# Kernel tuning notes

Measured on AMD Instinct MI355X. Metric: run time of the kernel, lower is better.

## Reference

```python
import jax, jax.numpy as jnp
import numpy as np

B, T, C, H = 2, 2048, 1024, 16
D = C // H  # head dim = 64
NEG_MIN = jnp.finfo(jnp.float32).min


def setup_inputs() -> dict:
    key = jax.random.key(0)
    ks = jax.random.split(key, 5)
    std = 0.02
    return {
        "x": jax.random.normal(ks[0], (B, T, C), dtype=jnp.float32),
        "Wq": std * jax.random.normal(ks[1], (C, C), dtype=jnp.float32),
        "bq": jnp.zeros((C,), dtype=jnp.float32),
        "Wk": std * jax.random.normal(ks[2], (C, C), dtype=jnp.float32),
        "bk": jnp.zeros((C,), dtype=jnp.float32),
        "Wv": std * jax.random.normal(ks[3], (C, C), dtype=jnp.float32),
        "bv": jnp.zeros((C,), dtype=jnp.float32),
        "Wo": (std / np.sqrt(24.0)) * jax.random.normal(ks[4], (C, C), dtype=jnp.float32),
        "bo": jnp.zeros((C,), dtype=jnp.float32),
    }


def reference(x, Wq, bq, Wk, bk, Wv, bv, Wo, bo):
    # QKV projections -> (B, H, T, D)
    def proj(W, b):
        return (x @ W + b).reshape(B, T, H, D).transpose(0, 2, 1, 3)

    q = proj(Wq, bq)
    k = proj(Wk, bk)
    v = proj(Wv, bv)

    # full scores (B, H, T, T), causal mask, softmax
    attn = jnp.einsum("bhqd,bhkd->bhqk", q, k) / jnp.sqrt(jnp.float32(D))
    mask = jnp.tril(jnp.ones((T, T), dtype=bool))[None, None]
    attn = jnp.where(mask, attn, NEG_MIN)
    scores = jax.nn.softmax(attn, axis=-1)

    out = jnp.einsum("bhqk,bhkd->bhqd", scores, v)
    out = out.transpose(0, 2, 1, 3).reshape(B, T, C)
    return out @ Wo + bo
```

## Files before the change

kernel.cpp:

```cpp
#include <hip/hip_runtime.h>
#include <stdint.h>
#include <stddef.h>


#define B_SZ 2
#define T_SZ 2048
#define C_SZ 1024
#define H_SZ 16
#define D_SZ 64
#define M_SZ (B_SZ * T_SZ)
#define BHTD (B_SZ * H_SZ * T_SZ * D_SZ)
#define CC (C_SZ * C_SZ)

typedef __attribute__((ext_vector_type(8))) __bf16 bf16x8;
typedef __attribute__((ext_vector_type(4))) float f32x4;
typedef __attribute__((ext_vector_type(16))) float f32x16;

__device__ __forceinline__ unsigned short f2bf(float f) {
    union { float f; unsigned u; } v; v.f = f;
    v.u += 0x7fffu + ((v.u >> 16) & 1u);
    return (unsigned short)(v.u >> 16);
}

__device__ __forceinline__ unsigned pkbf(float lo, float hi_) {
    union { unsigned u; __bf16 h[2]; } r;
    r.h[0] = (__bf16)lo; r.h[1] = (__bf16)hi_;
    return r.u;
}

__device__ __forceinline__ void load_lds16(const unsigned short* g, unsigned short* l) {
    __builtin_amdgcn_global_load_lds(
        (const __attribute__((address_space(1))) void*)g,
        (__attribute__((address_space(3))) void*)l, 16, 0, 0);
}


__global__ void cvt_x_kernel(const float4* __restrict__ in, ushort4* __restrict__ out, int n4) {
    int stride = gridDim.x * blockDim.x;
    for (int i = blockIdx.x * blockDim.x + threadIdx.x; i < n4; i += stride) {
        float4 v = in[i];
        ushort4 o;
        o.x = f2bf(v.x); o.y = f2bf(v.y); o.z = f2bf(v.z); o.w = f2bf(v.w);
        out[i] = o;
    }
}

__global__ __launch_bounds__(256) void transpose_cvt_kernel(
    const float* __restrict__ W0, const float* __restrict__ W1,
    const float* __restrict__ W2, const float* __restrict__ W3,
    unsigned short* __restrict__ T0, unsigned short* __restrict__ T1,
    unsigned short* __restrict__ T2, unsigned short* __restrict__ T3)
{
    __shared__ float tile[32][33];
    const float* W; unsigned short* Wt;
    switch (blockIdx.z) {
        case 0: W = W0; Wt = T0; break;
        case 1: W = W1; Wt = T1; break;
        case 2: W = W2; Wt = T2; break;
        default: W = W3; Wt = T3; break;
    }
    const int tx = threadIdx.x, ty = threadIdx.y;
    const int n0 = blockIdx.x * 32, k0 = blockIdx.y * 32;
    #pragma unroll
    for (int i = 0; i < 4; i++)
        tile[ty + i * 8][tx] = W[(size_t)(k0 + ty + i * 8) * C_SZ + n0 + tx];
    __syncthreads();
    #pragma unroll
    for (int i = 0; i < 4; i++)
        Wt[(size_t)(n0 + ty + i * 8) * C_SZ + k0 + tx] = f2bf(tile[tx][ty + i * 8]);
}

__global__ __launch_bounds__(256) void vt_kernel(
    const unsigned short* __restrict__ V, unsigned short* __restrict__ Vt)
{
    __shared__ unsigned short tile[32][33];
    const int bh = blockIdx.z;
    const int t0 = blockIdx.x * 32, d0 = blockIdx.y * 32;
    const unsigned short* src = V + (size_t)bh * T_SZ * D_SZ;
    unsigned short* dst = Vt + (size_t)bh * T_SZ * D_SZ;
    const int tx = threadIdx.x, ty = threadIdx.y;
    #pragma unroll
    for (int i = 0; i < 4; i++)
        tile[ty + i * 8][tx] = src[(size_t)(t0 + ty + i * 8) * D_SZ + d0 + tx];
    __syncthreads();
    #pragma unroll
    for (int i = 0; i < 4; i++)
        dst[(size_t)(d0 + ty + i * 8) * T_SZ + t0 + tx] = tile[tx][ty + i * 8];
}


__device__ __forceinline__ void gemm_tile_core(
    const unsigned short* __restrict__ A,
    const unsigned short* __restrict__ Bt,
    unsigned short* As, unsigned short* Bs,
    int m0, int n0, f32x4 acc[4][4])
{
    const int tid = threadIdx.x;
    const int lane = tid & 63;
    const int w = tid >> 6;
    const int l15 = lane & 15, lg = lane >> 4;
    const int wr = (w >> 1) * 64, wc = (w & 1) * 64;

    const unsigned short* Ag0 = A + (size_t)(m0 + (tid >> 2)) * C_SZ + (tid & 3) * 8;
    const unsigned short* Ag1 = Ag0 + (size_t)64 * C_SZ;
    const unsigned short* Bg0 = Bt + (size_t)(n0 + (tid >> 2)) * C_SZ + (tid & 3) * 8;
    const unsigned short* Bg1 = Bg0 + (size_t)64 * C_SZ;
    unsigned short* As0 = As + w * 512;
    unsigned short* As1 = As + 2048 + w * 512;
    unsigned short* Bs0 = Bs + w * 512;
    unsigned short* Bs1 = Bs + 2048 + w * 512;

    for (int k0 = 0; k0 < C_SZ; k0 += 32) {
        load_lds16(Ag0 + k0, As0);
        load_lds16(Ag1 + k0, As1);
        load_lds16(Bg0 + k0, Bs0);
        load_lds16(Bg1 + k0, Bs1);
        __syncthreads();
        bf16x8 af[4], bfv[4];
        const bf16x8* Ap = (const bf16x8*)As;
        const bf16x8* Bp = (const bf16x8*)Bs;
        #pragma unroll
        for (int m = 0; m < 4; m++) af[m] = Ap[(wr + m * 16 + l15) * 4 + lg];
        #pragma unroll
        for (int n = 0; n < 4; n++) bfv[n] = Bp[(wc + n * 16 + l15) * 4 + lg];
        #pragma unroll
        for (int m = 0; m < 4; m++)
            #pragma unroll
            for (int n = 0; n < 4; n++)
                acc[m][n] = __builtin_amdgcn_mfma_f32_16x16x32_bf16(af[m], bfv[n], acc[m][n], 0, 0, 0);
        __syncthreads();
    }
}

__global__ __launch_bounds__(256) void gemm_qkv_kernel(
    const unsigned short* __restrict__ A,
    const unsigned short* __restrict__ WtBase,
    const float* __restrict__ bq, const float* __restrict__ bk, const float* __restrict__ bv,
    unsigned short* __restrict__ QKV, unsigned short* __restrict__ Vtmp)
{
    __shared__ unsigned short As[4096], Bs[4096];
    const int z = blockIdx.z;
    const unsigned short* Bt = WtBase + (size_t)z * CC;
    const float* bias = (z == 0) ? bq : (z == 1) ? bk : bv;
    const float scale = (z == 0) ? 0.18033688011112042f : 1.0f;
    unsigned short* Out = (z == 2) ? Vtmp : QKV + (size_t)z * BHTD;

    f32x4 acc[4][4];
    f32x4 zero4 = {0.f, 0.f, 0.f, 0.f};
    #pragma unroll
    for (int m = 0; m < 4; m++)
        #pragma unroll
        for (int n = 0; n < 4; n++) acc[m][n] = zero4;

    const int m0 = blockIdx.y * 128, n0 = blockIdx.x * 128;
    gemm_tile_core(A, Bt, As, Bs, m0, n0, acc);

    const int lane = threadIdx.x & 63;
    const int w = threadIdx.x >> 6;
    const int l15 = lane & 15, lg = lane >> 4;
    const int wr = (w >> 1) * 64, wc = (w & 1) * 64;
    #pragma unroll
    for (int n = 0; n < 4; n++) {
        const int col = n0 + wc + n * 16 + l15;
        const float bias_v = bias[col];
        const int h = col >> 6, d = col & 63;
        #pragma unroll
        for (int m = 0; m < 4; m++) {
            #pragma unroll
            for (int j = 0; j < 4; j++) {
                const int row = m0 + wr + m * 16 + lg * 4 + j;
                const int b = row >> 11, t = row & (T_SZ - 1);
                Out[(((size_t)(b * H_SZ + h)) * T_SZ + t) * D_SZ + d] =
                    f2bf((acc[m][n][j] + bias_v) * scale);
            }
        }
    }
}

__global__ __launch_bounds__(256) void gemm_out_kernel(
    const unsigned short* __restrict__ A,
    const unsigned short* __restrict__ Bt,
    const float* __restrict__ bo,
    float* __restrict__ Out)
{
    __shared__ unsigned short As[4096], Bs[4096];
    f32x4 acc[4][4];
    f32x4 zero4 = {0.f, 0.f, 0.f, 0.f};
    #pragma unroll
    for (int m = 0; m < 4; m++)
        #pragma unroll
        for (int n = 0; n < 4; n++) acc[m][n] = zero4;

    const int m0 = blockIdx.y * 128, n0 = blockIdx.x * 128;
    gemm_tile_core(A, Bt, As, Bs, m0, n0, acc);

    const int lane = threadIdx.x & 63;
    const int w = threadIdx.x >> 6;
    const int l15 = lane & 15, lg = lane >> 4;
    const int wr = (w >> 1) * 64, wc = (w & 1) * 64;
    #pragma unroll
    for (int n = 0; n < 4; n++) {
        const int col = n0 + wc + n * 16 + l15;
        const float bias_v = bo[col];
        #pragma unroll
        for (int m = 0; m < 4; m++) {
            #pragma unroll
            for (int j = 0; j < 4; j++) {
                const int row = m0 + wr + m * 16 + lg * 4 + j;
                Out[(size_t)row * C_SZ + col] = acc[m][n][j] + bias_v;
            }
        }
    }
}

__global__ __launch_bounds__(256) void attn_fwd_kernel(
    const unsigned short* __restrict__ Q,
    const unsigned short* __restrict__ K,
    const unsigned short* __restrict__ Vt,
    unsigned short* __restrict__ O)
{
    const int idx = blockIdx.x;
    const int qt = (idx < 256) ? (15 - (idx >> 5)) : ((idx - 256) >> 5);
    const int bh = idx & 31;
    const int w = threadIdx.x >> 6;
    const int lane = threadIdx.x & 63;
    const int l31 = lane & 31, hi = lane >> 5;
    const int qw = qt * 128 + 32 * w;

    const unsigned short* Qh = Q + (size_t)bh * T_SZ * D_SZ;
    const unsigned short* Kh = K + (size_t)bh * T_SZ * D_SZ;
    const unsigned short* Vh = Vt + (size_t)bh * T_SZ * D_SZ;

    __shared__ __align__(16) unsigned short smem[16384];

    const int c0 = w * 64 + lane;
    const int row0 = c0 >> 3;
    const int sw0 = (c0 & 7) ^ (row0 & 7);
    const int koff0 = row0 * 64 + sw0 * 8;
    const int voff0 = row0 * T_SZ + sw0 * 8;
    const int ldsb0 = w * 512;

    bf16x8 qf[4];
    #pragma unroll
    for (int j = 0; j < 4; j++)
        qf[j] = *(const bf16x8*)&Qh[(size_t)(qw + l31) * D_SZ + j * 16 + 8 * hi];

    f32x16 acc[2];
    #pragma unroll
    for (int r = 0; r < 16; r++) { acc[0][r] = 0.f; acc[1][r] = 0.f; }
    float mrun = -3.0e38f, lrun = 0.f;

    const int tlast = (qw + 31) >> 6;
    const int ntb = 2 * qt + 2;
    const int qrow = qw + l31;
    const int swl = l31 & 7;

    load_lds16(Kh + koff0, smem + ldsb0);
    load_lds16(Kh + koff0 + 2048, smem + 2048 + ldsb0);
    load_lds16(Vh + voff0, smem + 4096 + ldsb0);
    load_lds16(Vh + voff0 + 32 * T_SZ, smem + 6144 + ldsb0);

    for (int tt = 0; tt < ntb; ++tt) {
        if (tt + 1 < ntb) {
            unsigned short* Bd = smem + ((tt + 1) & 1) * 8192;
            const unsigned short* Kt = Kh + (size_t)(tt + 1) * 64 * D_SZ;
            const unsigned short* Vtt = Vh + (tt + 1) * 64;
            load_lds16(Kt + koff0, Bd + ldsb0);
            load_lds16(Kt + koff0 + 2048, Bd + 2048 + ldsb0);
            load_lds16(Vtt + voff0, Bd + 4096 + ldsb0);
            load_lds16(Vtt + voff0 + 32 * T_SZ, Bd + 6144 + ldsb0);
            asm volatile("s_waitcnt vmcnt(4)" ::: "memory");
        } else {
            asm volatile("s_waitcnt vmcnt(0)" ::: "memory");
        }
        __builtin_amdgcn_s_barrier();

        if (tt <= tlast) {
            const unsigned short* Ks = smem + (tt & 1) * 8192;
            const unsigned short* Vs = Ks + 4096;
            const int k0 = tt * 64;

            f32x16 s[2];
            #pragma unroll
            for (int kb = 0; kb < 2; ++kb) {
                bf16x8 kf[4];
                #pragma unroll
                for (int j = 0; j < 4; ++j) {
                    const int ch = (j * 2 + hi) ^ swl;
                    kf[j] = *(const bf16x8*)&Ks[(kb * 32 + l31) * 64 + ch * 8];
                }
                f32x16 sc;
                #pragma unroll
                for (int r = 0; r < 16; r++) sc[r] = 0.f;
                #pragma unroll
                for (int j = 0; j < 4; ++j)
                    sc = __builtin_amdgcn_mfma_f32_32x32x16_bf16(kf[j], qf[j], sc, 0, 0, 0);
                s[kb] = sc;
            }

            if (k0 + 63 > qw) {
                #pragma unroll
                for (int kb = 0; kb < 2; ++kb)
                    #pragma unroll
                    for (int r = 0; r < 16; ++r) {
                        const int kv = k0 + kb * 32 + (r & 3) + 8 * (r >> 2) + 4 * hi;
                        s[kb][r] = (kv > qrow) ? -3.0e38f : s[kb][r];
                    }
            }

            float pm = s[0][0];
            #pragma unroll
            for (int r = 1; r < 16; r++) pm = fmaxf(pm, s[0][r]);
            #pragma unroll
            for (int r = 0; r < 16; r++) pm = fmaxf(pm, s[1][r]);
            pm = fmaxf(pm, __shfl_xor(pm, 32));

            if (!__all(pm <= mrun + 8.0f)) {
                const float mnew = fmaxf(mrun, pm);
                const float al = exp2f(mrun - mnew);
                lrun *= al;
                #pragma unroll
                for (int r = 0; r < 16; r++) { acc[0][r] *= al; acc[1][r] *= al; }
                mrun = mnew;
            }

            float ps = 0.f;
            #pragma unroll
            for (int kb = 0; kb < 2; ++kb)
                #pragma unroll
                for (int r = 0; r < 16; r++) { s[kb][r] = exp2f(s[kb][r] - mrun); ps += s[kb][r]; }
            ps += __shfl_xor(ps, 32);
            lrun += ps;

            bf16x8 pf[2][2];
            #pragma unroll
            for (int kb = 0; kb < 2; ++kb) {
                #pragma unroll
                for (int ksl = 0; ksl < 2; ++ksl) {
                    unsigned a0 = pkbf(s[kb][8 * ksl + 0], s[kb][8 * ksl + 1]);
                    unsigned a1 = pkbf(s[kb][8 * ksl + 2], s[kb][8 * ksl + 3]);
                    unsigned b0 = pkbf(s[kb][8 * ksl + 4], s[kb][8 * ksl + 5]);
                    unsigned b1 = pkbf(s[kb][8 * ksl + 6], s[kb][8 * ksl + 7]);
                    asm volatile("v_permlane32_swap_b32 %0, %1" : "+v"(a0), "+v"(b0));
                    asm volatile("v_permlane32_swap_b32 %0, %1" : "+v"(a1), "+v"(b1));
                    union { unsigned u[4]; bf16x8 v; } fr;
                    fr.u[0] = a0; fr.u[1] = a1; fr.u[2] = b0; fr.u[3] = b1;
                    pf[kb][ksl] = fr.v;
                }
            }

            #pragma unroll
            for (int dt = 0; dt < 2; ++dt)
                #pragma unroll
                for (int kb = 0; kb < 2; ++kb)
                    #pragma unroll
                    for (int ksl = 0; ksl < 2; ++ksl) {
                        const int ks = kb * 2 + ksl;
                        const int ch = (ks * 2 + hi) ^ swl;
                        const bf16x8 vf = *(const bf16x8*)&Vs[(dt * 32 + l31) * 64 + ch * 8];
                        acc[dt] = __builtin_amdgcn_mfma_f32_32x32x16_bf16(vf, pf[kb][ksl], acc[dt], 0, 0, 0);
                    }
        }
        __builtin_amdgcn_s_barrier();
    }

    unsigned short* ot = smem + w * 2304;
    const float inv = 1.0f / lrun;
    #pragma unroll
    for (int g = 0; g < 4; g++) {
        ushort4 wa, wb;
        wa.x = f2bf(acc[0][4 * g + 0] * inv); wa.y = f2bf(acc[0][4 * g + 1] * inv);
        wa.z = f2bf(acc[0][4 * g + 2] * inv); wa.w = f2bf(acc[0][4 * g + 3] * inv);
        wb.x = f2bf(acc[1][4 * g + 0] * inv); wb.y = f2bf(acc[1][4 * g + 1] * inv);
        wb.z = f2bf(acc[1][4 * g + 2] * inv); wb.w = f2bf(acc[1][4 * g + 3] * inv);
        *(ushort4*)&ot[l31 * 72 + 8 * g + 4 * hi] = wa;
        *(ushort4*)&ot[l31 * 72 + 32 + 8 * g + 4 * hi] = wb;
    }
    const int b = bh >> 4, h = bh & 15;
    #pragma unroll
    for (int pss = 0; pss < 4; pss++) {
        const int q = pss * 8 + (lane >> 3);
        const uint4 val = *(const uint4*)&ot[q * 72 + (lane & 7) * 8];
        *(uint4*)&O[((size_t)(b * T_SZ + qw + q)) * C_SZ + h * D_SZ + (lane & 7) * 8] = val;
    }
}


extern "C" void kernel_launch(void* const* d_in, const int* in_sizes, int n_in,
                              void* d_out, int out_size, void* d_ws, size_t ws_size,
                              hipStream_t stream)
{
    const float* x  = (const float*)d_in[0];
    const float* Wq = (const float*)d_in[1];
    const float* bq = (const float*)d_in[2];
    const float* Wk = (const float*)d_in[3];
    const float* bk = (const float*)d_in[4];
    const float* Wv = (const float*)d_in[5];
    const float* bv = (const float*)d_in[6];
    const float* Wo = (const float*)d_in[7];
    const float* bo = (const float*)d_in[8];

    uint8_t* ws = (uint8_t*)d_ws;
    unsigned short* XB   = (unsigned short*)(ws);
    unsigned short* WT   = (unsigned short*)(ws + (8u  << 20));
    unsigned short* QKV  = (unsigned short*)(ws + (16u << 20));
    unsigned short* Vtmp = (unsigned short*)(ws + (40u << 20));

    cvt_x_kernel<<<2048, 256, 0, stream>>>((const float4*)x, (ushort4*)XB, M_SZ * C_SZ / 4);
    transpose_cvt_kernel<<<dim3(32, 32, 4), dim3(32, 8), 0, stream>>>(
        Wq, Wk, Wv, Wo, WT, WT + CC, WT + 2 * (size_t)CC, WT + 3 * (size_t)CC);
    gemm_qkv_kernel<<<dim3(8, 32, 3), 256, 0, stream>>>(XB, WT, bq, bk, bv, QKV, Vtmp);
    vt_kernel<<<dim3(64, 2, 32), dim3(32, 8), 0, stream>>>(Vtmp, QKV + 2 * (size_t)BHTD);
    attn_fwd_kernel<<<512, 256, 0, stream>>>(
        QKV, QKV + BHTD, QKV + 2 * (size_t)BHTD, Vtmp);
    gemm_out_kernel<<<dim3(8, 32), 256, 0, stream>>>(Vtmp, WT + 3 * (size_t)CC, bo, (float*)d_out);
}
```

Baseline: 131.8 us.

## Retile output GEMM to 64x128, flatten QKV grid, tree-reduce softmax max/sum

```diff
diff --git a/kernel.cpp b/kernel.cpp
--- a/kernel.cpp
+++ b/kernel.cpp
@@ -139,7 +139,7 @@
     unsigned short* __restrict__ QKV, unsigned short* __restrict__ Vtmp)
 {
     __shared__ unsigned short As[4096], Bs[4096];
-    const int z = blockIdx.z;
+    const int z = blockIdx.x >> 3;
     const unsigned short* Bt = WtBase + (size_t)z * CC;
     const float* bias = (z == 0) ? bq : (z == 1) ? bk : bv;
     const float scale = (z == 0) ? 0.18033688011112042f : 1.0f;
@@ -152,7 +152,7 @@
         #pragma unroll
         for (int n = 0; n < 4; n++) acc[m][n] = zero4;
 
-    const int m0 = blockIdx.y * 128, n0 = blockIdx.x * 128;
+    const int m0 = blockIdx.y * 128, n0 = (blockIdx.x & 7) * 128;
     gemm_tile_core(A, Bt, As, Bs, m0, n0, acc);
 
     const int lane = threadIdx.x & 63;
@@ -183,30 +183,57 @@
     const float* __restrict__ bo,
     float* __restrict__ Out)
 {
-    __shared__ unsigned short As[4096], Bs[4096];
-    f32x4 acc[4][4];
+    __shared__ unsigned short As[2048], Bs[4096];
+    const int tid = threadIdx.x;
+    const int lane = tid & 63;
+    const int w = tid >> 6;
+    const int l15 = lane & 15, lg = lane >> 4;
+    const int wc = w * 32;
+    const int m0 = blockIdx.y * 64, n0 = blockIdx.x * 128;
+
+    const unsigned short* Ag  = A + (size_t)(m0 + (tid >> 2)) * C_SZ + (tid & 3) * 8;
+    const unsigned short* Bg0 = Bt + (size_t)(n0 + (tid >> 2)) * C_SZ + (tid & 3) * 8;
+    const unsigned short* Bg1 = Bg0 + (size_t)64 * C_SZ;
+    unsigned short* As0 = As + w * 512;
+    unsigned short* Bs0 = Bs + w * 512;
+    unsigned short* Bs1 = Bs + 2048 + w * 512;
+
+    f32x4 acc[4][2];
     f32x4 zero4 = {0.f, 0.f, 0.f, 0.f};
     #pragma unroll
     for (int m = 0; m < 4; m++)
         #pragma unroll
-        for (int n = 0; n < 4; n++) acc[m][n] = zero4;
-
-    const int m0 = blockIdx.y * 128, n0 = blockIdx.x * 128;
-    gemm_tile_core(A, Bt, As, Bs, m0, n0, acc);
-
-    const int lane = threadIdx.x & 63;
-    const int w = threadIdx.x >> 6;
-    const int l15 = lane & 15, lg = lane >> 4;
-    const int wr = (w >> 1) * 64, wc = (w & 1) * 64;
-    #pragma unroll
-    for (int n = 0; n < 4; n++) {
+        for (int n = 0; n < 2; n++) acc[m][n] = zero4;
+
+    for (int k0 = 0; k0 < C_SZ; k0 += 32) {
+        load_lds16(Ag + k0, As0);
+        load_lds16(Bg0 + k0, Bs0);
+        load_lds16(Bg1 + k0, Bs1);
+        __syncthreads();
+        bf16x8 af[4], bfv[2];
+        const bf16x8* Ap = (const bf16x8*)As;
+        const bf16x8* Bp = (const bf16x8*)Bs;
+        #pragma unroll
+        for (int m = 0; m < 4; m++) af[m] = Ap[(m * 16 + l15) * 4 + lg];
+        #pragma unroll
+        for (int n = 0; n < 2; n++) bfv[n] = Bp[(wc + n * 16 + l15) * 4 + lg];
+        #pragma unroll
+        for (int m = 0; m < 4; m++)
+            #pragma unroll
+            for (int n = 0; n < 2; n++)
+                acc[m][n] = __builtin_amdgcn_mfma_f32_16x16x32_bf16(af[m], bfv[n], acc[m][n], 0, 0, 0);
+        __syncthreads();
+    }
+
+    #pragma unroll
+    for (int n = 0; n < 2; n++) {
         const int col = n0 + wc + n * 16 + l15;
         const float bias_v = bo[col];
         #pragma unroll
         for (int m = 0; m < 4; m++) {
             #pragma unroll
             for (int j = 0; j < 4; j++) {
-                const int row = m0 + wr + m * 16 + lg * 4 + j;
+                const int row = m0 + m * 16 + lg * 4 + j;
                 Out[(size_t)row * C_SZ + col] = acc[m][n][j] + bias_v;
             }
         }
@@ -308,12 +335,14 @@
                     }
             }
 
-            float pm = s[0][0];
-            #pragma unroll
-            for (int r = 1; r < 16; r++) pm = fmaxf(pm, s[0][r]);
-            #pragma unroll
-            for (int r = 0; r < 16; r++) pm = fmaxf(pm, s[1][r]);
-            pm = fmaxf(pm, __shfl_xor(pm, 32));
+            float t16[16];
+            #pragma unroll
+            for (int i = 0; i < 16; i++) t16[i] = fmaxf(s[0][i], s[1][i]);
+            #pragma unroll
+            for (int st = 8; st >= 1; st >>= 1)
+                #pragma unroll
+                for (int i = 0; i < st; i++) t16[i] = fmaxf(t16[i], t16[i + st]);
+            const float pm = fmaxf(t16[0], __shfl_xor(t16[0], 32));
 
             if (!__all(pm <= mrun + 8.0f)) {
                 const float mnew = fmaxf(mrun, pm);
@@ -324,13 +353,18 @@
                 mrun = mnew;
             }
 
-            float ps = 0.f;
             #pragma unroll
             for (int kb = 0; kb < 2; ++kb)
                 #pragma unroll
-                for (int r = 0; r < 16; r++) { s[kb][r] = exp2f(s[kb][r] - mrun); ps += s[kb][r]; }
-            ps += __shfl_xor(ps, 32);
-            lrun += ps;
+                for (int r = 0; r < 16; r++) s[kb][r] = exp2f(s[kb][r] - mrun);
+            float a16[16];
+            #pragma unroll
+            for (int i = 0; i < 16; i++) a16[i] = s[0][i] + s[1][i];
+            #pragma unroll
+            for (int st = 8; st >= 1; st >>= 1)
+                #pragma unroll
+                for (int i = 0; i < st; i++) a16[i] += a16[i + st];
+            lrun += a16[0] + __shfl_xor(a16[0], 32);
 
             bf16x8 pf[2][2];
             #pragma unroll
@@ -409,9 +443,9 @@
     cvt_x_kernel<<<2048, 256, 0, stream>>>((const float4*)x, (ushort4*)XB, M_SZ * C_SZ / 4);
     transpose_cvt_kernel<<<dim3(32, 32, 4), dim3(32, 8), 0, stream>>>(
         Wq, Wk, Wv, Wo, WT, WT + CC, WT + 2 * (size_t)CC, WT + 3 * (size_t)CC);
-    gemm_qkv_kernel<<<dim3(8, 32, 3), 256, 0, stream>>>(XB, WT, bq, bk, bv, QKV, Vtmp);
+    gemm_qkv_kernel<<<dim3(24, 32), 256, 0, stream>>>(XB, WT, bq, bk, bv, QKV, Vtmp);
     vt_kernel<<<dim3(64, 2, 32), dim3(32, 8), 0, stream>>>(Vtmp, QKV + 2 * (size_t)BHTD);
     attn_fwd_kernel<<<512, 256, 0, stream>>>(
         QKV, QKV + BHTD, QKV + 2 * (size_t)BHTD, Vtmp);
-    gemm_out_kernel<<<dim3(8, 32), 256, 0, stream>>>(Vtmp, WT + 3 * (size_t)CC, bo, (float*)d_out);
-}
+    gemm_out_kernel<<<dim3(8, 64), 256, 0, stream>>>(Vtmp, WT + 3 * (size_t)CC, bo, (float*)d_out);
+}
```

Result: faster. 129.0 us (-2.1%).
